# Optimization experiments

Hardware: AMD Instinct MI355X
Metric: run time of the kernel (lower is better)

The kernel has to match this reference:

```python
import jax, jax.numpy as jnp
import numpy as np
from jax import lax

B, C, H, W = 16, 128, 64, 64
AUX = 2 * 128 + 20 + 1  # hybrid: edge(128)+seg(128)+pred_edge(1)+pred_seg(20)
PATCHES = [(2, 2), (4, 4)]


def conv1x1(x, w, b):
    # w: [O, I]
    return jnp.einsum('bchw,oc->bohw', x, w) + b[None, :, None, None]


def conv3x3(x, w, b, pad, dil=1):
    y = lax.conv_general_dilated(x, w, (1, 1), [(pad, pad), (pad, pad)],
                                 rhs_dilation=(dil, dil),
                                 dimension_numbers=('NCHW', 'OIHW', 'NCHW'))
    return y + b[None, :, None, None]


def layernorm_chw(x, eps=1e-5):
    # LayerNorm over [C,H,W] per sample, no affine
    mu = x.mean(axis=(1, 2, 3), keepdims=True)
    var = ((x - mu) ** 2).mean(axis=(1, 2, 3), keepdims=True)
    return (x - mu) / jnp.sqrt(var + eps)


def adn(x, aux, ew, eb, sw, sb, bw, bb):
    a = conv1x1(aux, ew, eb)
    gamma = conv1x1(a, sw, sb)
    beta = conv1x1(jnp.concatenate([x, a], axis=1), bw, bb)
    return layernorm_chw(x) * gamma + beta


def window_attn(q, k, v, ph, pw):
    b, dk, h, w = q.shape
    oh, ow = h // ph, w // pw

    def patch(t):  # [b,dk,h,w] -> [b, oh*ow, dk*ph*pw]
        t = t.reshape(b, dk, oh, ph, ow, pw)
        return t.transpose(0, 2, 4, 1, 3, 5).reshape(b, oh * ow, dk * ph * pw)

    Q, K, V = patch(q), patch(k), patch(v)
    scale = 1.0 / jnp.sqrt(jnp.asarray(Q.shape[-1], Q.dtype))
    scores = jnp.einsum('bnd,bmd->bnm', Q, K) * scale
    y = jnp.einsum('bnm,bmd->bnd', jax.nn.softmax(scores, axis=-1), V)
    y = y.reshape(b, oh, ow, dk, ph, pw).transpose(0, 3, 1, 4, 2, 5).reshape(b, dk, h, w)
    return y


def mssa_forward(p):
    (x, edge, seg, pred_edge, pred_seg,
     q_w, q_b, k_w, k_b, v_w, v_b,
     d1_embed_w, d1_embed_b, d1_scale_w, d1_scale_b, d1_bias_w, d1_bias_b,
     d2_embed_w, d2_embed_b, d2_scale_w, d2_scale_b, d2_bias_w, d2_bias_b,
     sc_w, sc_b, bi1_w, bi1_b, bi2_w, bi2_b) = p

    aux = jnp.concatenate([edge, seg, pred_edge, pred_seg], axis=1)

    q = adn(conv1x1(x, q_w, q_b), aux, d1_embed_w, d1_embed_b, d1_scale_w, d1_scale_b, d1_bias_w, d1_bias_b)
    k = adn(conv1x1(x, k_w, k_b), aux, d1_embed_w, d1_embed_b, d1_scale_w, d1_scale_b, d1_bias_w, d1_bias_b)
    v = adn(conv1x1(x, v_w, v_b), aux, d1_embed_w, d1_embed_b, d1_scale_w, d1_scale_b, d1_bias_w, d1_bias_b)

    qs = jnp.split(q, len(PATCHES), axis=1)
    ks = jnp.split(k, len(PATCHES), axis=1)
    vs = jnp.split(v, len(PATCHES), axis=1)
    outs = [window_attn(qs[i], ks[i], vs[i], PATCHES[i][1], PATCHES[i][0]) for i in range(len(PATCHES))]

    mid = x + jnp.concatenate(outs, axis=1)
    o = adn(mid, aux, d2_embed_w, d2_embed_b, d2_scale_w, d2_scale_b, d2_bias_w, d2_bias_b)
    gamma = jnp.tanh(conv3x3(o, sc_w, sc_b, pad=1))
    beta = conv3x3(jax.nn.gelu(conv3x3(o, bi1_w, bi1_b, pad=2, dil=2), approximate=False), bi2_w, bi2_b, pad=1)
    return mid * gamma + beta


def setup_inputs() -> dict:
    key = jax.random.key(0)
    ks = iter(jax.random.split(key, 40))
    nrm = lambda shape, s=1.0: jax.random.normal(next(ks), shape, jnp.float32) * s
    P = 0.02  # param init scale
    inp = {
        'x': nrm((B, C, H, W)),
        'edge': nrm((B, 128, H, W)),
        'seg': nrm((B, 128, H, W)),
        'pred_edge': jax.random.uniform(next(ks), (B, 1, H, W), jnp.float32),
        'pred_seg': jax.random.uniform(next(ks), (B, 20, H, W), jnp.float32),
        'q_w': nrm((C, C), P), 'q_b': jnp.zeros((C,), jnp.float32),
        'k_w': nrm((C, C), P), 'k_b': jnp.zeros((C,), jnp.float32),
        'v_w': nrm((C, C), P), 'v_b': jnp.zeros((C,), jnp.float32),
        'd1_embed_w': nrm((C, AUX), P), 'd1_embed_b': jnp.zeros((C,), jnp.float32),
        'd1_scale_w': nrm((C, C), P), 'd1_scale_b': jnp.ones((C,), jnp.float32),
        'd1_bias_w': nrm((C, 2 * C), P), 'd1_bias_b': jnp.zeros((C,), jnp.float32),
        'd2_embed_w': nrm((C, AUX), P), 'd2_embed_b': jnp.zeros((C,), jnp.float32),
        'd2_scale_w': nrm((C, C), P), 'd2_scale_b': jnp.ones((C,), jnp.float32),
        'd2_bias_w': nrm((C, 2 * C), P), 'd2_bias_b': jnp.zeros((C,), jnp.float32),
        'sc_w': nrm((C, C, 3, 3), P), 'sc_b': jnp.zeros((C,), jnp.float32),
        'bi1_w': nrm((C, C, 3, 3), P), 'bi1_b': jnp.zeros((C,), jnp.float32),
        'bi2_w': nrm((C, C, 3, 3), P), 'bi2_b': jnp.zeros((C,), jnp.float32),
    }
    return inp


def reference(x, edge, seg, pred_edge, pred_seg,
              q_w, q_b, k_w, k_b, v_w, v_b,
              d1_embed_w, d1_embed_b, d1_scale_w, d1_scale_b, d1_bias_w, d1_bias_b,
              d2_embed_w, d2_embed_b, d2_scale_w, d2_scale_b, d2_bias_w, d2_bias_b,
              sc_w, sc_b, bi1_w, bi1_b, bi2_w, bi2_b):
    return mssa_forward((x, edge, seg, pred_edge, pred_seg,
                         q_w, q_b, k_w, k_b, v_w, v_b,
                         d1_embed_w, d1_embed_b, d1_scale_w, d1_scale_b, d1_bias_w, d1_bias_b,
                         d2_embed_w, d2_embed_b, d2_scale_w, d2_scale_b, d2_bias_w, d2_bias_b,
                         sc_w, sc_b, bi1_w, bi1_b, bi2_w, bi2_b))
```

## Files before the change

kernel.cpp:

```cpp
#include <hip/hip_runtime.h>
#include <cstdint>

typedef unsigned short ushort_t;
typedef unsigned int uint_t;
typedef __attribute__((ext_vector_type(8))) short short8;
typedef __attribute__((ext_vector_type(4))) float f32x4;

#define MFMA16(a, b, c) __builtin_amdgcn_mfma_f32_16x16x32_bf16((a), (b), (c), 0, 0, 0)
#define SWZ(c, r) ((((c) + ((r) >> 2)) & 3))
#define INV_N 1.9073486328125e-6f

struct P4 { ushort_t* p[4]; };
struct B4 { const float* b[4]; };

__device__ __forceinline__ ushort_t f2bf(float f) {
    uint_t u = __builtin_bit_cast(uint_t, f);
    u += 0x7FFFu + ((u >> 16) & 1u);
    return (ushort_t)(u >> 16);
}
__device__ __forceinline__ float bf2f(ushort_t h) {
    return __builtin_bit_cast(float, (uint_t)h << 16);
}

__global__ __launch_bounds__(256) void prep_w(
    ushort_t* wb, const float* qw, const float* kw, const float* vw,
    const float* ew1, const float* ew2, const float* sw1, const float* sw2,
    const float* bw1, const float* bw2,
    const float* scw, const float* b1w, const float* b2w)
{
    int idx = blockIdx.x * 256 + threadIdx.x;
    if (idx >= 663552) return;
    float v;
    if (idx < 49152) {
        int z = idx >> 14, r = idx & 16383;
        v = (z == 0 ? qw : z == 1 ? kw : vw)[r];
    } else if (idx < 122880) {
        int j = idx - 49152; int z = j / 36864; int jj = j - z * 36864;
        int o = jj / 288, k = jj - o * 288;
        v = (k < 277) ? (z ? ew2 : ew1)[o * 277 + k] : 0.f;
    } else if (idx < 155648) {
        int j = idx - 122880; int z = j >> 14;
        v = (z ? sw2 : sw1)[j & 16383];
    } else if (idx < 221184) {
        int j = idx - 155648; int z = j >> 15;
        v = (z ? bw2 : bw1)[j & 32767];
    } else {
        int j = idx - 221184;
        const float* src = j < 147456 ? scw : j < 294912 ? b1w : b2w;
        j = j % 147456;
        int tap = j >> 14, r = (j >> 7) & 127, c = j & 127;
        v = src[r * 1152 + c * 9 + tap];
    }
    wb[idx] = f2bf(v);
}

__global__ __launch_bounds__(256) void combine_w(ushort_t* wc, const ushort_t* wb)
{
    __shared__ float ews[128 * 33];
    __shared__ ushort_t Ws[128 * 130];
    int z = blockIdx.y, nt = blockIdx.x, n0 = nt * 32;
    int t = threadIdx.x;
    const ushort_t* wew = wb + 49152;
    const ushort_t* wsw = wb + 122880;
    const ushort_t* wbw = wb + 155648;
    const ushort_t* W; int wstr, wof;
    if (z == 0)      { W = wsw;         wstr = 128; wof = 0; }
    else if (z == 1) { W = wbw;         wstr = 256; wof = 128; }
    else if (z == 2) { W = wsw + 16384; wstr = 128; wof = 0; }
    else             { W = wbw + 32768; wstr = 256; wof = 128; }
    const ushort_t* E = wew + (z >= 2 ? 36864 : 0);
    for (int s = t; s < 16384; s += 256) {
        int c = s & 127, o = s >> 7;
        Ws[c * 130 + o] = W[o * wstr + wof + c];
    }
    for (int s = t; s < 4096; s += 256) {
        int c = s >> 5, n = s & 31;
        ews[c * 33 + n] = bf2f(E[c * 288 + n0 + n]);
    }
    __syncthreads();
    int o = t & 127, nh = t >> 7;
    float acc[16];
#pragma unroll
    for (int i = 0; i < 16; ++i) acc[i] = 0.f;
    for (int c = 0; c < 128; ++c) {
        float wv = bf2f(Ws[c * 130 + o]);
#pragma unroll
        for (int i = 0; i < 16; ++i) acc[i] += wv * ews[c * 33 + nh * 16 + i];
    }
#pragma unroll
    for (int i = 0; i < 16; ++i)
        wc[(size_t)(z * 128 + o) * 288 + n0 + nh * 16 + i] = f2bf(acc[i]);
}

__global__ __launch_bounds__(512) void combine_bias(
    float* bc, const float* sw1, const float* bw1, const float* sw2, const float* bw2,
    const float* eb1, const float* eb2, const float* sb1, const float* bb1,
    const float* sb2, const float* bb2)
{
    int t = threadIdx.x; int z = t >> 7, o = t & 127;
    const float* W; int wstr, wof; const float* eb; float add;
    if (z == 0)      { W = sw1; wstr = 128; wof = 0;   eb = eb1; add = sb1[o]; }
    else if (z == 1) { W = bw1; wstr = 256; wof = 128; eb = eb1; add = bb1[o]; }
    else if (z == 2) { W = sw2; wstr = 128; wof = 0;   eb = eb2; add = sb2[o]; }
    else             { W = bw2; wstr = 256; wof = 128; eb = eb2; add = bb2[o]; }
    float s = add;
    for (int c = 0; c < 128; ++c) s += W[o * wstr + wof + c] * eb[c];
    bc[t] = s;
}

__global__ __launch_bounds__(256) void transp_x(const float* __restrict__ x, ushort_t* __restrict__ xT)
{
    __shared__ ushort_t tile[64 * 130];
    int b = blockIdx.y, p0 = blockIdx.x * 64;
    int t = threadIdx.x;
#pragma unroll
    for (int i = 0; i < 8; ++i) {
        int s = t + i * 256;
        int c = s >> 4, p4 = (s & 15) * 4;
        float4 f = *(const float4*)(x + ((size_t)(b * 128 + c) << 12) + p0 + p4);
        tile[(p4 + 0) * 130 + c] = f2bf(f.x);
        tile[(p4 + 1) * 130 + c] = f2bf(f.y);
        tile[(p4 + 2) * 130 + c] = f2bf(f.z);
        tile[(p4 + 3) * 130 + c] = f2bf(f.w);
    }
    __syncthreads();
#pragma unroll
    for (int i = 0; i < 4; ++i) {
        int s = t + i * 256;
        int p = s >> 4, c8 = (s & 15) * 8;
        ushort_t v[8];
#pragma unroll
        for (int e = 0; e < 8; ++e) v[e] = tile[p * 130 + c8 + e];
        uint4 ov = {(uint_t)v[0] | ((uint_t)v[1] << 16), (uint_t)v[2] | ((uint_t)v[3] << 16),
                    (uint_t)v[4] | ((uint_t)v[5] << 16), (uint_t)v[6] | ((uint_t)v[7] << 16)};
        *(uint4*)(xT + ((size_t)(b * 4096) + p0 + p) * 128 + c8) = ov;
    }
}

__global__ __launch_bounds__(256) void transp_aux(const float* __restrict__ edge, const float* __restrict__ seg,
                                                  const float* __restrict__ pe, const float* __restrict__ ps,
                                                  ushort_t* __restrict__ auxT)
{
    __shared__ ushort_t tile[64 * 292];
    int b = blockIdx.y, p0 = blockIdx.x * 64;
    int t = threadIdx.x;
#pragma unroll
    for (int i = 0; i < 18; ++i) {
        int s = t + i * 256;
        int c = s >> 4, p4 = (s & 15) * 4;
        float4 f = {0.f, 0.f, 0.f, 0.f};
        if (c < 128)       f = *(const float4*)(edge + ((size_t)(b * 128 + c) << 12) + p0 + p4);
        else if (c < 256)  f = *(const float4*)(seg + ((size_t)(b * 128 + c - 128) << 12) + p0 + p4);
        else if (c == 256) f = *(const float4*)(pe + ((size_t)b << 12) + p0 + p4);
        else if (c < 277)  f = *(const float4*)(ps + ((size_t)(b * 20 + c - 257) << 12) + p0 + p4);
        tile[(p4 + 0) * 292 + c] = f2bf(f.x);
        tile[(p4 + 1) * 292 + c] = f2bf(f.y);
        tile[(p4 + 2) * 292 + c] = f2bf(f.z);
        tile[(p4 + 3) * 292 + c] = f2bf(f.w);
    }
    __syncthreads();
#pragma unroll
    for (int i = 0; i < 9; ++i) {
        int s = t + i * 256;
        int p = s / 36, c8 = (s % 36) * 8;
        ushort_t v[8];
#pragma unroll
        for (int e = 0; e < 8; ++e) v[e] = tile[p * 292 + c8 + e];
        uint4 ov = {(uint_t)v[0] | ((uint_t)v[1] << 16), (uint_t)v[2] | ((uint_t)v[3] << 16),
                    (uint_t)v[4] | ((uint_t)v[5] << 16), (uint_t)v[6] | ((uint_t)v[7] << 16)};
        *(uint4*)(auxT + ((size_t)(b * 4096) + p0 + p) * 288 + c8) = ov;
    }
}

template <int EP>
__global__ __launch_bounds__(256) void gemm_conv(
    const ushort_t* bA, int Kb1, size_t zBoff,
    const ushort_t* wA, int wstride, int wAperZ, int NK,
    B4 bias4, P4 out4, const ushort_t* gT, const ushort_t* betT,
    float* stats, int dostats)
{
    constexpr int LDSZ = (EP == 2) ? 33792 : 16448;
    __shared__ char lds[LDSZ];
    int b = blockIdx.y, bx = blockIdx.x, z = blockIdx.z;
    int t = threadIdx.x, lane = t & 63, w = t >> 6;
    int wm = w & 1, wn = w >> 1, lo = lane & 15, quad = lane >> 4;
    const ushort_t* wAz = wA + (wAperZ ? (size_t)z * 128 * wstride : 0);
    const ushort_t* bAz = bA + (size_t)z * zBoff;
    ushort_t* outp = out4.p[z];
    size_t bbase = (size_t)b * 4096;
    int y0 = 0, x0 = 0;
    if (EP == 2) { y0 = (bx >> 1) * 4; x0 = (bx & 1) * 32; }

    f32x4 acc[4][4];
#pragma unroll
    for (int i = 0; i < 4; ++i)
#pragma unroll
        for (int j = 0; j < 4; ++j) acc[i][j] = (f32x4){0.f, 0.f, 0.f, 0.f};

    int r0 = t >> 2, c0 = t & 3, r1 = r0 + 64;
    int gp0, gp1;
    if (EP == 2) {
        gp0 = (y0 + (r0 >> 5)) * 64 + x0 + (r0 & 31);
        gp1 = (y0 + (r1 >> 5)) * 64 + x0 + (r1 & 31);
    } else {
        gp0 = bx * 128 + r0;
        gp1 = bx * 128 + r1;
    }
    const ushort_t* bRow0 = bAz + (bbase + gp0) * Kb1;
    const ushort_t* bRow1 = bAz + (bbase + gp1) * Kb1;
    uint4 pfA0 = *(const uint4*)(wAz + (size_t)r0 * wstride + c0 * 8);
    uint4 pfA1 = *(const uint4*)(wAz + (size_t)r1 * wstride + c0 * 8);
    uint4 pfB0 = *(const uint4*)(bRow0 + c0 * 8);
    uint4 pfB1 = *(const uint4*)(bRow1 + c0 * 8);
    for (int ck = 0; ck < NK; ++ck) {
        __syncthreads();
        *(uint4*)(lds + r0 * 64 + SWZ(c0, r0) * 16) = pfA0;
        *(uint4*)(lds + r1 * 64 + SWZ(c0, r1) * 16) = pfA1;
        *(uint4*)(lds + 8192 + r0 * 64 + SWZ(c0, r0) * 16) = pfB0;
        *(uint4*)(lds + 8192 + r1 * 64 + SWZ(c0, r1) * 16) = pfB1;
        __syncthreads();
        if (ck + 1 < NK) {
            int k0 = (ck + 1) * 32;
            pfA0 = *(const uint4*)(wAz + (size_t)r0 * wstride + k0 + c0 * 8);
            pfA1 = *(const uint4*)(wAz + (size_t)r1 * wstride + k0 + c0 * 8);
            pfB0 = *(const uint4*)(bRow0 + k0 + c0 * 8);
            pfB1 = *(const uint4*)(bRow1 + k0 + c0 * 8);
        }
        short8 af[4];
#pragma unroll
        for (int mt = 0; mt < 4; ++mt) {
            int row = wm * 64 + mt * 16 + lo;
            af[mt] = *(const short8*)(lds + row * 64 + SWZ(quad, row) * 16);
        }
#pragma unroll
        for (int nt = 0; nt < 4; ++nt) {
            int n = wn * 64 + nt * 16 + lo;
            short8 bf = *(const short8*)(lds + 8192 + n * 64 + SWZ(quad, n) * 16);
#pragma unroll
            for (int mt = 0; mt < 4; ++mt) acc[mt][nt] = MFMA16(af[mt], bf, acc[mt][nt]);
        }
    }

    float mean = 0.f, rstd = 0.f;
    if (EP >= 2) {
        int slot = (EP == 3) ? 3 : z;
        float s0 = stats[(slot * 16 + b) * 2], s1 = stats[(slot * 16 + b) * 2 + 1];
        mean = s0 * INV_N;
        rstd = rsqrtf(fmaxf(s1 * INV_N - mean * mean, 0.f) + 1e-5f);
    }
    float lsum = 0.f, lss = 0.f;
    if (EP == 2) {
        __syncthreads();
        ushort_t* Cs = (ushort_t*)lds;
#pragma unroll
        for (int mt = 0; mt < 4; ++mt)
#pragma unroll
            for (int nt = 0; nt < 4; ++nt) {
                int oo0 = wm * 64 + mt * 16 + quad * 4;
                int pp = wn * 64 + nt * 16 + lo;
                int gp = (y0 + (pp >> 5)) * 64 + x0 + (pp & 31);
                size_t tbase = (bbase + gp) * 128 + oo0;
                ushort4 tv = *(const ushort4*)(bAz + tbase);
                ushort4 gv = *(const ushort4*)(gT + tbase);
                ushort4 bv = *(const ushort4*)(betT + tbase);
#pragma unroll
                for (int r = 0; r < 4; ++r) {
                    float v = acc[mt][nt][r] + bf2f((&bv.x)[r])
                            + (bf2f((&tv.x)[r]) - mean) * rstd * bf2f((&gv.x)[r]);
                    Cs[(oo0 + r) * 132 + pp] = f2bf(v);
                }
            }
        __syncthreads();
        if (z < 2) {
            for (int s = t; s < 1024; s += 256) {
                int n_l = s >> 5, fq = s & 31;
                int ypair = n_l >> 4, xp = n_l & 15;
                ushort_t tmp[8];
#pragma unroll
                for (int e = 0; e < 8; ++e) {
                    int f = fq * 8 + e;
                    int c = f >> 2, py = (f >> 1) & 1, px = f & 1;
                    tmp[e] = Cs[c * 132 + (ypair * 2 + py) * 32 + xp * 2 + px];
                }
                int n = ((y0 >> 1) + ypair) * 32 + (x0 >> 1) + xp;
                uint4 ov = {(uint_t)tmp[0] | ((uint_t)tmp[1] << 16), (uint_t)tmp[2] | ((uint_t)tmp[3] << 16),
                            (uint_t)tmp[4] | ((uint_t)tmp[5] << 16), (uint_t)tmp[6] | ((uint_t)tmp[7] << 16)};
                *(uint4*)(outp + ((size_t)(b * 1024 + n) << 8) + fq * 8) = ov;
            }
            for (int s = t; s < 1024; s += 256) {
                int n_l = s >> 7, fq = s & 127;
                ushort_t tmp[8];
#pragma unroll
                for (int e = 0; e < 8; ++e) {
                    int f = fq * 8 + e;
                    int c = f >> 4, py = (f >> 2) & 3, px = f & 3;
                    tmp[e] = Cs[(64 + c) * 132 + py * 32 + n_l * 4 + px];
                }
                int n = (y0 >> 2) * 16 + (x0 >> 2) + n_l;
                uint4 ov = {(uint_t)tmp[0] | ((uint_t)tmp[1] << 16), (uint_t)tmp[2] | ((uint_t)tmp[3] << 16),
                            (uint_t)tmp[4] | ((uint_t)tmp[5] << 16), (uint_t)tmp[6] | ((uint_t)tmp[7] << 16)};
                *(uint4*)(outp + 4194304u + ((size_t)(b * 256 + n) << 10) + fq * 8) = ov;
            }
        } else {
            for (int s = t; s < 2048; s += 256) {
                int f = s >> 3, j = s & 7;
                int ypair = j >> 2, xq = j & 3;
                int c = f >> 2, py = (f >> 1) & 1, px = f & 1;
                ushort_t tmp[4];
#pragma unroll
                for (int i2 = 0; i2 < 4; ++i2)
                    tmp[i2] = Cs[c * 132 + (ypair * 2 + py) * 32 + (xq * 4 + i2) * 2 + px];
                int m0 = ((y0 >> 1) + ypair) * 32 + (x0 >> 1) + xq * 4;
                uint2 ov = {(uint_t)tmp[0] | ((uint_t)tmp[1] << 16), (uint_t)tmp[2] | ((uint_t)tmp[3] << 16)};
                *(uint2*)(outp + ((size_t)(b * 256 + f) << 10) + m0) = ov;
            }
            for (int s = t; s < 2048; s += 256) {
                int f = s >> 1, j = s & 1;
                int c = f >> 4, py = (f >> 2) & 3, px = f & 3;
                ushort_t tmp[4];
#pragma unroll
                for (int i2 = 0; i2 < 4; ++i2)
                    tmp[i2] = Cs[(64 + c) * 132 + py * 32 + (j * 4 + i2) * 4 + px];
                int m0 = (y0 >> 2) * 16 + (x0 >> 2) + j * 4;
                uint2 ov = {(uint_t)tmp[0] | ((uint_t)tmp[1] << 16), (uint_t)tmp[2] | ((uint_t)tmp[3] << 16)};
                *(uint2*)(outp + 4194304u + ((size_t)(b * 1024 + f) << 8) + m0) = ov;
            }
        }
    } else {
#pragma unroll
        for (int mt = 0; mt < 4; ++mt)
#pragma unroll
            for (int nt = 0; nt < 4; ++nt) {
                int oo0 = wm * 64 + mt * 16 + quad * 4;
                int pp = wn * 64 + nt * 16 + lo;
                size_t tbase = (bbase + bx * 128 + pp) * 128 + oo0;
                float vv[4];
                if (EP == 0) {
#pragma unroll
                    for (int r = 0; r < 4; ++r) vv[r] = acc[mt][nt][r] + bias4.b[z][oo0 + r];
                    if (dostats) {
#pragma unroll
                        for (int r = 0; r < 4; ++r) { lsum += vv[r]; lss += vv[r] * vv[r]; }
                    }
                } else {
                    ushort4 tv = *(const ushort4*)(bAz + tbase);
                    ushort4 gv = *(const ushort4*)(gT + tbase);
                    ushort4 bv = *(const ushort4*)(betT + tbase);
#pragma unroll
                    for (int r = 0; r < 4; ++r)
                        vv[r] = acc[mt][nt][r] + bf2f((&bv.x)[r])
                              + (bf2f((&tv.x)[r]) - mean) * rstd * bf2f((&gv.x)[r]);
                }
                ushort4 st = {f2bf(vv[0]), f2bf(vv[1]), f2bf(vv[2]), f2bf(vv[3])};
                *(ushort4*)(outp + tbase) = st;
            }
    }
    if (EP == 0 && dostats) {
#pragma unroll
        for (int o2 = 32; o2 >= 1; o2 >>= 1) { lsum += __shfl_xor(lsum, o2); lss += __shfl_xor(lss, o2); }
        __syncthreads();
        float* red = (float*)lds;
        if (lane == 0) { red[w * 2] = lsum; red[w * 2 + 1] = lss; }
        __syncthreads();
        if (t == 0) {
            atomicAdd(&stats[(z * 16 + b) * 2], red[0] + red[2] + red[4] + red[6]);
            atomicAdd(&stats[(z * 16 + b) * 2 + 1], red[1] + red[3] + red[5] + red[7]);
        }
    }
}

template <int EP>
__global__ __launch_bounds__(256) void gemm_attn(
    const ushort_t* A, size_t aBS, const ushort_t* Bm, size_t bBS,
    int Ka, int NK, float scale,
    ushort_t* sout, size_t soBS, int soNb,
    const ushort_t* xT, ushort_t* midT, float* stats)
{
    constexpr int LDSZ = (EP >= 1) ? 33792 : 16448;
    __shared__ char lds[LDSZ];
    int b = blockIdx.z, my = blockIdx.y, nx = blockIdx.x;
    int t = threadIdx.x, lane = t & 63, w = t >> 6;
    int wm = w & 1, wn = w >> 1, lo = lane & 15, quad = lane >> 4;

    f32x4 acc[4][4];
#pragma unroll
    for (int i = 0; i < 4; ++i)
#pragma unroll
        for (int j = 0; j < 4; ++j) acc[i][j] = (f32x4){0.f, 0.f, 0.f, 0.f};

    const ushort_t* Ab = A + b * aBS + (size_t)(my * 128) * Ka;
    const ushort_t* Bb = Bm + b * bBS + (size_t)(nx * 128) * Ka;
    int r0 = t >> 2, c0 = t & 3, r1 = r0 + 64;
    uint4 pfA0 = *(const uint4*)(Ab + (size_t)r0 * Ka + c0 * 8);
    uint4 pfA1 = *(const uint4*)(Ab + (size_t)r1 * Ka + c0 * 8);
    uint4 pfB0 = *(const uint4*)(Bb + (size_t)r0 * Ka + c0 * 8);
    uint4 pfB1 = *(const uint4*)(Bb + (size_t)r1 * Ka + c0 * 8);
    for (int ck = 0; ck < NK; ++ck) {
        __syncthreads();
        *(uint4*)(lds + r0 * 64 + SWZ(c0, r0) * 16) = pfA0;
        *(uint4*)(lds + r1 * 64 + SWZ(c0, r1) * 16) = pfA1;
        *(uint4*)(lds + 8192 + r0 * 64 + SWZ(c0, r0) * 16) = pfB0;
        *(uint4*)(lds + 8192 + r1 * 64 + SWZ(c0, r1) * 16) = pfB1;
        __syncthreads();
        if (ck + 1 < NK) {
            int k0 = (ck + 1) * 32;
            pfA0 = *(const uint4*)(Ab + (size_t)r0 * Ka + k0 + c0 * 8);
            pfA1 = *(const uint4*)(Ab + (size_t)r1 * Ka + k0 + c0 * 8);
            pfB0 = *(const uint4*)(Bb + (size_t)r0 * Ka + k0 + c0 * 8);
            pfB1 = *(const uint4*)(Bb + (size_t)r1 * Ka + k0 + c0 * 8);
        }
        short8 af[4];
#pragma unroll
        for (int mt = 0; mt < 4; ++mt) {
            int row = wm * 64 + mt * 16 + lo;
            af[mt] = *(const short8*)(lds + row * 64 + SWZ(quad, row) * 16);
        }
#pragma unroll
        for (int nt = 0; nt < 4; ++nt) {
            int n = wn * 64 + nt * 16 + lo;
            short8 bf = *(const short8*)(lds + 8192 + n * 64 + SWZ(quad, n) * 16);
#pragma unroll
            for (int mt = 0; mt < 4; ++mt) acc[mt][nt] = MFMA16(af[mt], bf, acc[mt][nt]);
        }
    }

    if (EP == 0) {
#pragma unroll
        for (int mt = 0; mt < 4; ++mt)
#pragma unroll
            for (int nt = 0; nt < 4; ++nt)
#pragma unroll
                for (int reg = 0; reg < 4; ++reg) {
                    int rr = my * 128 + wm * 64 + mt * 16 + quad * 4 + reg;
                    int cc = nx * 128 + wn * 64 + nt * 16 + lo;
                    sout[(size_t)b * soBS + (size_t)rr * soNb + cc] = f2bf(acc[mt][nt][reg] * scale);
                }
        return;
    }
    __syncthreads();
    ushort_t* Cs = (ushort_t*)lds;
#pragma unroll
    for (int mt = 0; mt < 4; ++mt)
#pragma unroll
        for (int nt = 0; nt < 4; ++nt)
#pragma unroll
            for (int reg = 0; reg < 4; ++reg) {
                int r_l = wm * 64 + mt * 16 + quad * 4 + reg;
                int c_l = wn * 64 + nt * 16 + lo;
                Cs[r_l * 132 + c_l] = f2bf(acc[mt][nt][reg]);
            }
    __syncthreads();
    float lsum = 0.f, lss = 0.f;
    for (int s = t; s < 4096; s += 256) {
        int sp, r_l, cbase, pybit, pxbit;
        if (EP == 1) {
            int sp_l = s >> 3, cj = s & 7;
            int y_l = sp_l >> 6, xv = sp_l & 63;
            r_l = (y_l >> 1) * 32 + (xv >> 1);
            sp = (my * 8 + y_l) * 64 + xv;
            cbase = nx * 32 + cj * 4;
            pybit = (y_l & 1) * 2 + (xv & 1);
            pxbit = 4;
        } else {
            int sp_l = s >> 1, cj = s & 1;
            int y_l = sp_l >> 6, xv = sp_l & 63;
            r_l = (y_l >> 2) * 16 + (xv >> 2);
            sp = (my * 32 + y_l) * 64 + xv;
            cbase = 64 + nx * 8 + cj * 4;
            pybit = (y_l & 3) * 4 + (xv & 3);
            pxbit = 16;
        }
        size_t base = ((size_t)(b * 4096) + sp) * 128 + cbase;
        ushort4 xv4 = *(const ushort4*)(xT + base);
        int c_l0 = (EP == 1) ? (cbase - nx * 32) * 4 + pybit : (cbase - 64 - nx * 8) * 16 + pybit;
        ushort_t o4[4];
#pragma unroll
        for (int ci = 0; ci < 4; ++ci) {
            float vm = bf2f(Cs[r_l * 132 + c_l0 + ci * pxbit]) + bf2f((&xv4.x)[ci]);
            o4[ci] = f2bf(vm);
            lsum += vm; lss += vm * vm;
        }
        ushort4 st = {o4[0], o4[1], o4[2], o4[3]};
        *(ushort4*)(midT + base) = st;
    }
#pragma unroll
    for (int o2 = 32; o2 >= 1; o2 >>= 1) { lsum += __shfl_xor(lsum, o2); lss += __shfl_xor(lss, o2); }
    __syncthreads();
    float* red = (float*)lds;
    if (lane == 0) { red[w * 2] = lsum; red[w * 2 + 1] = lss; }
    __syncthreads();
    if (t == 0) {
        atomicAdd(&stats[(3 * 16 + b) * 2], red[0] + red[2] + red[4] + red[6]);
        atomicAdd(&stats[(3 * 16 + b) * 2 + 1], red[1] + red[3] + red[5] + red[7]);
    }
}

__global__ __launch_bounds__(256) void softmax_k(ushort_t* SP)
{
    int wid = blockIdx.x * 4 + (threadIdx.x >> 6);
    int lane = threadIdx.x & 63;
    ushort_t* row;
    int PL;
    if (wid < 16384) { row = SP + ((size_t)wid << 10); PL = 16; }
    else { int r2 = wid - 16384; row = SP + 16777216u + ((size_t)r2 << 8); PL = 4; }
    float v[16];
    float mx = -1e30f;
    for (int i = 0; i < PL; ++i) { v[i] = bf2f(row[lane + (i << 6)]); mx = fmaxf(mx, v[i]); }
#pragma unroll
    for (int o = 32; o >= 1; o >>= 1) mx = fmaxf(mx, __shfl_xor(mx, o));
    float sum = 0.f;
    for (int i = 0; i < PL; ++i) { v[i] = __expf(v[i] - mx); sum += v[i]; }
#pragma unroll
    for (int o = 32; o >= 1; o >>= 1) sum += __shfl_xor(sum, o);
    float inv = 1.f / sum;
    for (int i = 0; i < PL; ++i) row[lane + (i << 6)] = f2bf(v[i] * inv);
}

__global__ __launch_bounds__(512) void conv3x3_dual(
    const ushort_t* __restrict__ inT, const ushort_t* __restrict__ wtA, const ushort_t* __restrict__ wtB,
    const float* __restrict__ biasA, const float* __restrict__ biasB,
    ushort_t* __restrict__ outA, ushort_t* __restrict__ outB)
{
    __shared__ char lds[24576 + 8 * 68 * 64];
    char* Braw = lds + 24576;
    int b = blockIdx.y, z = blockIdx.z;
    int dil = 1 + z;
    int NRr = 4 + 2 * dil;
    const ushort_t* wt = z ? wtB : wtA;
    const float* bias = z ? biasB : biasA;
    ushort_t* out = z ? outB : outA;
    int y0 = blockIdx.x * 4;
    int t = threadIdx.x, lane = t & 63, w = t >> 6;
    int wm = w & 1, wn = w >> 1, lo = lane & 15, quad = lane >> 4;

    f32x4 acc[4][4];
#pragma unroll
    for (int i = 0; i < 4; ++i)
#pragma unroll
        for (int j = 0; j < 4; ++j) acc[i][j] = (f32x4){0.f, 0.f, 0.f, 0.f};

    for (int cc = 0; cc < 4; ++cc) {
        __syncthreads();
        int NSLOT = NRr * 68 * 4;
        for (int s = t; s < NSLOT; s += 512) {
            int c4 = s & 3;
            int pr = s >> 2;
            int xx = pr % 68, rr = pr / 68;
            int ys = y0 - dil + rr;
            int ix = xx - dil;
            uint4 v = {0u, 0u, 0u, 0u};
            if (ys >= 0 && ys < 64 && (unsigned)ix < 64u)
                v = *(const uint4*)(inT + (size_t)(b * 4096 + ys * 64 + ix) * 128 + cc * 32 + c4 * 8);
            *(uint4*)(Braw + pr * 64 + SWZ(c4, pr) * 16) = v;
        }
        for (int ky = 0; ky < 3; ++ky) {
            __syncthreads();
            for (int s = t; s < 1536; s += 512) {
                int kx = s >> 9, r = (s >> 2) & 127, c = s & 3;
                uint4 v = *(const uint4*)(wt + ((size_t)((ky * 3 + kx) * 128 + r) << 7) + cc * 32 + c * 8);
                *(uint4*)(lds + kx * 8192 + r * 64 + SWZ(c, r) * 16) = v;
            }
            __syncthreads();
#pragma unroll
            for (int kx = 0; kx < 3; ++kx) {
                short8 af[4];
#pragma unroll
                for (int mt = 0; mt < 4; ++mt) {
                    int row = wm * 64 + mt * 16 + lo;
                    af[mt] = *(const short8*)(lds + kx * 8192 + row * 64 + SWZ(quad, row) * 16);
                }
#pragma unroll
                for (int nt = 0; nt < 4; ++nt) {
                    int n = wn * 64 + nt * 16 + lo;
                    int pr = ((n >> 6) + ky * dil) * 68 + (n & 63) + kx * dil;
                    short8 bf = *(const short8*)(Braw + pr * 64 + SWZ(quad, pr) * 16);
#pragma unroll
                    for (int mt = 0; mt < 4; ++mt) acc[mt][nt] = MFMA16(af[mt], bf, acc[mt][nt]);
                }
            }
        }
    }
#pragma unroll
    for (int mt = 0; mt < 4; ++mt)
#pragma unroll
        for (int nt = 0; nt < 4; ++nt) {
            int oo0 = wm * 64 + mt * 16 + quad * 4;
            int pp = wn * 64 + nt * 16 + lo;
            int sp = (y0 + (pp >> 6)) * 64 + (pp & 63);
            size_t tbase = ((size_t)(b * 4096) + sp) * 128 + oo0;
            ushort4 st;
#pragma unroll
            for (int r = 0; r < 4; ++r) {
                float v = acc[mt][nt][r] + bias[oo0 + r];
                if (z == 0) v = tanhf(v);
                else        v = 0.5f * v * (1.f + erff(v * 0.70710678118654752f));
                (&st.x)[r] = f2bf(v);
            }
            *(ushort4*)(out + tbase) = st;
        }
}

__global__ __launch_bounds__(512) void conv3x3_final(
    const ushort_t* __restrict__ inT, const ushort_t* __restrict__ wt, const float* __restrict__ bias,
    float* __restrict__ out, const ushort_t* __restrict__ midT, const ushort_t* __restrict__ g3T)
{
    __shared__ char lds[24576 + 6 * 68 * 64];
    char* Braw = lds + 24576;
    int b = blockIdx.y;
    int y0 = blockIdx.x * 4;
    int t = threadIdx.x, lane = t & 63, w = t >> 6;
    int wm = w & 1, wn = w >> 1, lo = lane & 15, quad = lane >> 4;

    f32x4 acc[4][4];
#pragma unroll
    for (int i = 0; i < 4; ++i)
#pragma unroll
        for (int j = 0; j < 4; ++j) acc[i][j] = (f32x4){0.f, 0.f, 0.f, 0.f};

    for (int cc = 0; cc < 4; ++cc) {
        __syncthreads();
        for (int s = t; s < 1632; s += 512) {
            int c4 = s & 3;
            int pr = s >> 2;
            int xx = pr % 68, rr = pr / 68;
            int ys = y0 - 1 + rr;
            int ix = xx - 1;
            uint4 v = {0u, 0u, 0u, 0u};
            if (ys >= 0 && ys < 64 && (unsigned)ix < 64u)
                v = *(const uint4*)(inT + (size_t)(b * 4096 + ys * 64 + ix) * 128 + cc * 32 + c4 * 8);
            *(uint4*)(Braw + pr * 64 + SWZ(c4, pr) * 16) = v;
        }
        for (int ky = 0; ky < 3; ++ky) {
            __syncthreads();
            for (int s = t; s < 1536; s += 512) {
                int kx = s >> 9, r = (s >> 2) & 127, c = s & 3;
                uint4 v = *(const uint4*)(wt + ((size_t)((ky * 3 + kx) * 128 + r) << 7) + cc * 32 + c * 8);
                *(uint4*)(lds + kx * 8192 + r * 64 + SWZ(c, r) * 16) = v;
            }
            __syncthreads();
#pragma unroll
            for (int kx = 0; kx < 3; ++kx) {
                short8 af[4];
#pragma unroll
                for (int mt = 0; mt < 4; ++mt) {
                    int row = wm * 64 + mt * 16 + lo;
                    af[mt] = *(const short8*)(lds + kx * 8192 + row * 64 + SWZ(quad, row) * 16);
                }
#pragma unroll
                for (int nt = 0; nt < 4; ++nt) {
                    int n = wn * 64 + nt * 16 + lo;
                    int pr = ((n >> 6) + ky) * 68 + (n & 63) + kx;
                    short8 bf = *(const short8*)(Braw + pr * 64 + SWZ(quad, pr) * 16);
#pragma unroll
                    for (int mt = 0; mt < 4; ++mt) acc[mt][nt] = MFMA16(af[mt], bf, acc[mt][nt]);
                }
            }
        }
    }
#pragma unroll
    for (int mt = 0; mt < 4; ++mt)
#pragma unroll
        for (int nt = 0; nt < 4; ++nt) {
            int oo0 = wm * 64 + mt * 16 + quad * 4;
            int pp = wn * 64 + nt * 16 + lo;
            int sp = (y0 + (pp >> 6)) * 64 + (pp & 63);
            size_t tbase = ((size_t)(b * 4096) + sp) * 128 + oo0;
            ushort4 mv = *(const ushort4*)(midT + tbase);
            ushort4 gv = *(const ushort4*)(g3T + tbase);
#pragma unroll
            for (int r = 0; r < 4; ++r) {
                int oo = oo0 + r;
                size_t off = ((size_t)(b * 128 + oo) << 12) + sp;
                out[off] = bf2f((&mv.x)[r]) * bf2f((&gv.x)[r]) + acc[mt][nt][r] + bias[oo];
            }
        }
}

extern "C" void kernel_launch(void* const* d_in, const int* in_sizes, int n_in,
                              void* d_out, int out_size, void* d_ws, size_t ws_size,
                              hipStream_t stream)
{
    const float* x    = (const float*)d_in[0];
    const float* edge = (const float*)d_in[1];
    const float* seg  = (const float*)d_in[2];
    const float* pe   = (const float*)d_in[3];
    const float* ps   = (const float*)d_in[4];
    const float* q_w  = (const float*)d_in[5];  const float* q_b  = (const float*)d_in[6];
    const float* k_w  = (const float*)d_in[7];  const float* k_b  = (const float*)d_in[8];
    const float* v_w  = (const float*)d_in[9];  const float* v_b  = (const float*)d_in[10];
    const float* d1_ew = (const float*)d_in[11]; const float* d1_eb = (const float*)d_in[12];
    const float* d1_sw = (const float*)d_in[13]; const float* d1_sb = (const float*)d_in[14];
    const float* d1_bw = (const float*)d_in[15]; const float* d1_bb = (const float*)d_in[16];
    const float* d2_ew = (const float*)d_in[17]; const float* d2_eb = (const float*)d_in[18];
    const float* d2_sw = (const float*)d_in[19]; const float* d2_sb = (const float*)d_in[20];
    const float* d2_bw = (const float*)d_in[21]; const float* d2_bb = (const float*)d_in[22];
    const float* sc_w  = (const float*)d_in[23]; const float* sc_b  = (const float*)d_in[24];
    const float* bi1_w = (const float*)d_in[25]; const float* bi1_b = (const float*)d_in[26];
    const float* bi2_w = (const float*)d_in[27]; const float* bi2_b = (const float*)d_in[28];

    char* ws = (char*)d_ws;
    ushort_t* wb = (ushort_t*)ws;
    ushort_t* wc = (ushort_t*)(ws + 1327360);
    float* bc    = (float*)(ws + 1622272);
    float* stats = (float*)(ws + 1624320);
    char* RA = ws + 1703936;
    char* RB = RA + 37748736;
    char* RC = RB + 16777216;
    char* RD = RC + 50331648;
    char* RE = RD + 16777216;
    char* RF = RE + 16777216;
    char* RG = RF + 16777216;
    char* RH = RG + 16777216;
    char* RI = RH + 33554432;

    ushort_t* auxT = (ushort_t*)RA;
    ushort_t* SP0  = (ushort_t*)RA;
    ushort_t* xT   = (ushort_t*)RB;
    ushort_t* q0T  = (ushort_t*)RC;
    ushort_t* midT = (ushort_t*)RC;
    ushort_t* oT   = (ushort_t*)(RC + 16777216);
    ushort_t* g1   = (ushort_t*)RD;
    ushort_t* g3   = (ushort_t*)RD;
    ushort_t* betA1= (ushort_t*)RE;
    ushort_t* g2   = (ushort_t*)RF;
    ushort_t* betA2= (ushort_t*)RG;
    ushort_t* Qp   = (ushort_t*)RH;
    ushort_t* Kp   = Qp + 8388608;
    ushort_t* VT   = (ushort_t*)RI;
    ushort_t* tT   = (ushort_t*)RI;
    const size_t ZB = 8388608;

    dim3 blk(256);

    hipMemsetAsync(stats, 0, 512, stream);
    prep_w<<<2592, blk, 0, stream>>>(wb, q_w, k_w, v_w, d1_ew, d2_ew, d1_sw, d2_sw, d1_bw, d2_bw, sc_w, bi1_w, bi2_w);
    combine_bias<<<1, 512, 0, stream>>>(bc, d1_sw, d1_bw, d2_sw, d2_bw, d1_eb, d2_eb, d1_sb, d1_bb, d2_sb, d2_bb);
    combine_w<<<dim3(9, 4), blk, 0, stream>>>(wc, wb);
    transp_x<<<dim3(64, 16), blk, 0, stream>>>(x, xT);
    transp_aux<<<dim3(64, 16), blk, 0, stream>>>(edge, seg, pe, ps, auxT);

    gemm_conv<0><<<dim3(32, 16, 4), blk, 0, stream>>>(auxT, 288, 0, wc, 288, 1, 9,
        B4{{bc, bc + 128, bc + 256, bc + 384}}, P4{{g1, betA1, g2, betA2}}, nullptr, nullptr, stats, 0);
    gemm_conv<0><<<dim3(32, 16, 3), blk, 0, stream>>>(xT, 128, 0, wb, 128, 1, 4,
        B4{{q_b, k_b, v_b, nullptr}}, P4{{q0T, q0T + ZB, q0T + 2 * ZB, nullptr}}, nullptr, nullptr, stats, 1);
    gemm_conv<2><<<dim3(32, 16, 3), blk, 0, stream>>>(q0T, 128, ZB, wb + 155648, 256, 0, 4,
        B4{{nullptr, nullptr, nullptr, nullptr}}, P4{{Qp, Kp, VT, nullptr}}, g1, betA1, stats, 0);

    gemm_attn<0><<<dim3(8, 8, 16), blk, 0, stream>>>(Qp, 262144, Kp, 262144, 256, 8, 0.0625f,
        SP0, 1048576, 1024, nullptr, nullptr, stats);
    gemm_attn<0><<<dim3(2, 2, 16), blk, 0, stream>>>(Qp + 4194304, 262144, Kp + 4194304, 262144, 1024, 32, 0.03125f,
        SP0 + 16777216, 65536, 256, nullptr, nullptr, stats);
    softmax_k<<<5120, blk, 0, stream>>>(SP0);
    gemm_attn<1><<<dim3(2, 8, 16), blk, 0, stream>>>(SP0, 1048576, VT, 262144, 1024, 32, 1.f,
        nullptr, 0, 0, xT, midT, stats);
    gemm_attn<2><<<dim3(8, 2, 16), blk, 0, stream>>>(SP0 + 16777216, 65536, VT + 4194304, 262144, 256, 8, 1.f,
        nullptr, 0, 0, xT, midT, stats);

    gemm_conv<3><<<dim3(32, 16, 1), blk, 0, stream>>>(midT, 128, 0, wb + 155648 + 32768, 256, 0, 4,
        B4{{nullptr, nullptr, nullptr, nullptr}}, P4{{oT, nullptr, nullptr, nullptr}}, g2, betA2, stats, 0);

    conv3x3_dual<<<dim3(16, 16, 2), dim3(512), 0, stream>>>(oT, wb + 221184, wb + 368640, sc_b, bi1_b, g3, tT);
    conv3x3_final<<<dim3(16, 16), dim3(512), 0, stream>>>(tT, wb + 516096, bi2_b, (float*)d_out, midT, g3);
}
```

Measured before the change: 694.5 us.

## Stage all nine conv taps per channel chunk and enlarge dual-conv row tile

Both 3x3 conv kernels now load the weights for all nine taps of a 32-channel chunk into LDS at once, so each chunk needs one barrier pair instead of one per ky row. The dual conv kernel also doubles its tile to 8 output rows with 1024-thread blocks, which halves the block count and spreads the halo and weight loads over more output rows. The cost is much larger LDS use (about 72KB of weights plus the halo tile), which caps how many blocks fit on a CU, and fewer blocks in the grid.

```diff
diff --git a/kernel.cpp b/kernel.cpp
--- a/kernel.cpp
+++ b/kernel.cpp
@@ -516,22 +516,22 @@
     for (int i = 0; i < PL; ++i) row[lane + (i << 6)] = f2bf(v[i] * inv);
 }
 
-__global__ __launch_bounds__(512) void conv3x3_dual(
+__global__ __launch_bounds__(1024) void conv3x3_dual(
     const ushort_t* __restrict__ inT, const ushort_t* __restrict__ wtA, const ushort_t* __restrict__ wtB,
     const float* __restrict__ biasA, const float* __restrict__ biasB,
     ushort_t* __restrict__ outA, ushort_t* __restrict__ outB)
 {
-    __shared__ char lds[24576 + 8 * 68 * 64];
-    char* Braw = lds + 24576;
+    __shared__ char lds[73728 + 12 * 68 * 64];
+    char* Braw = lds + 73728;
     int b = blockIdx.y, z = blockIdx.z;
     int dil = 1 + z;
-    int NRr = 4 + 2 * dil;
+    int NRr = 8 + 2 * dil;
     const ushort_t* wt = z ? wtB : wtA;
     const float* bias = z ? biasB : biasA;
     ushort_t* out = z ? outB : outA;
-    int y0 = blockIdx.x * 4;
+    int y0 = blockIdx.x * 8;
     int t = threadIdx.x, lane = t & 63, w = t >> 6;
-    int wm = w & 1, wn = w >> 1, lo = lane & 15, quad = lane >> 4;
+    int wm = w & 1, wr = w >> 1, lo = lane & 15, quad = lane >> 4;
 
     f32x4 acc[4][4];
 #pragma unroll
@@ -540,9 +540,14 @@
         for (int j = 0; j < 4; ++j) acc[i][j] = (f32x4){0.f, 0.f, 0.f, 0.f};
 
     for (int cc = 0; cc < 4; ++cc) {
-        __syncthreads();
-        int NSLOT = NRr * 68 * 4;
-        for (int s = t; s < NSLOT; s += 512) {
+        if (cc) __syncthreads();
+        for (int s = t; s < 4608; s += 1024) {
+            int tap = s >> 9, r = (s >> 2) & 127, c = s & 3;
+            uint4 v = *(const uint4*)(wt + ((size_t)(tap * 128 + r) << 7) + cc * 32 + c * 8);
+            *(uint4*)(lds + tap * 8192 + r * 64 + SWZ(c, r) * 16) = v;
+        }
+        int NSLOT = NRr * 272;
+        for (int s = t; s < NSLOT; s += 1024) {
             int c4 = s & 3;
             int pr = s >> 2;
             int xx = pr % 68, rr = pr / 68;
@@ -553,30 +558,22 @@
                 v = *(const uint4*)(inT + (size_t)(b * 4096 + ys * 64 + ix) * 128 + cc * 32 + c4 * 8);
             *(uint4*)(Braw + pr * 64 + SWZ(c4, pr) * 16) = v;
         }
-        for (int ky = 0; ky < 3; ++ky) {
-            __syncthreads();
-            for (int s = t; s < 1536; s += 512) {
-                int kx = s >> 9, r = (s >> 2) & 127, c = s & 3;
-                uint4 v = *(const uint4*)(wt + ((size_t)((ky * 3 + kx) * 128 + r) << 7) + cc * 32 + c * 8);
-                *(uint4*)(lds + kx * 8192 + r * 64 + SWZ(c, r) * 16) = v;
-            }
-            __syncthreads();
-#pragma unroll
-            for (int kx = 0; kx < 3; ++kx) {
-                short8 af[4];
-#pragma unroll
-                for (int mt = 0; mt < 4; ++mt) {
-                    int row = wm * 64 + mt * 16 + lo;
-                    af[mt] = *(const short8*)(lds + kx * 8192 + row * 64 + SWZ(quad, row) * 16);
-                }
-#pragma unroll
-                for (int nt = 0; nt < 4; ++nt) {
-                    int n = wn * 64 + nt * 16 + lo;
-                    int pr = ((n >> 6) + ky * dil) * 68 + (n & 63) + kx * dil;
-                    short8 bf = *(const short8*)(Braw + pr * 64 + SWZ(quad, pr) * 16);
-#pragma unroll
-                    for (int mt = 0; mt < 4; ++mt) acc[mt][nt] = MFMA16(af[mt], bf, acc[mt][nt]);
-                }
+        __syncthreads();
+#pragma unroll
+        for (int tap = 0; tap < 9; ++tap) {
+            int ky = tap / 3, kx = tap % 3;
+            short8 af[4];
+#pragma unroll
+            for (int mt = 0; mt < 4; ++mt) {
+                int row = wm * 64 + mt * 16 + lo;
+                af[mt] = *(const short8*)(lds + tap * 8192 + row * 64 + SWZ(quad, row) * 16);
+            }
+#pragma unroll
+            for (int nt = 0; nt < 4; ++nt) {
+                int pr = (wr + ky * dil) * 68 + nt * 16 + lo + kx * dil;
+                short8 bf = *(const short8*)(Braw + pr * 64 + SWZ(quad, pr) * 16);
+#pragma unroll
+                for (int mt = 0; mt < 4; ++mt) acc[mt][nt] = MFMA16(af[mt], bf, acc[mt][nt]);
             }
         }
     }
@@ -585,8 +582,8 @@
 #pragma unroll
         for (int nt = 0; nt < 4; ++nt) {
             int oo0 = wm * 64 + mt * 16 + quad * 4;
-            int pp = wn * 64 + nt * 16 + lo;
-            int sp = (y0 + (pp >> 6)) * 64 + (pp & 63);
+            int col = nt * 16 + lo;
+            int sp = (y0 + wr) * 64 + col;
             size_t tbase = ((size_t)(b * 4096) + sp) * 128 + oo0;
             ushort4 st;
 #pragma unroll
@@ -604,12 +601,12 @@
     const ushort_t* __restrict__ inT, const ushort_t* __restrict__ wt, const float* __restrict__ bias,
     float* __restrict__ out, const ushort_t* __restrict__ midT, const ushort_t* __restrict__ g3T)
 {
-    __shared__ char lds[24576 + 6 * 68 * 64];
-    char* Braw = lds + 24576;
+    __shared__ char lds[73728 + 6 * 68 * 64];
+    char* Braw = lds + 73728;
     int b = blockIdx.y;
     int y0 = blockIdx.x * 4;
     int t = threadIdx.x, lane = t & 63, w = t >> 6;
-    int wm = w & 1, wn = w >> 1, lo = lane & 15, quad = lane >> 4;
+    int wm = w & 1, wr = w >> 1, lo = lane & 15, quad = lane >> 4;
 
     f32x4 acc[4][4];
 #pragma unroll
@@ -618,7 +615,12 @@
         for (int j = 0; j < 4; ++j) acc[i][j] = (f32x4){0.f, 0.f, 0.f, 0.f};
 
     for (int cc = 0; cc < 4; ++cc) {
-        __syncthreads();
+        if (cc) __syncthreads();
+        for (int s = t; s < 4608; s += 512) {
+            int tap = s >> 9, r = (s >> 2) & 127, c = s & 3;
+            uint4 v = *(const uint4*)(wt + ((size_t)(tap * 128 + r) << 7) + cc * 32 + c * 8);
+            *(uint4*)(lds + tap * 8192 + r * 64 + SWZ(c, r) * 16) = v;
+        }
         for (int s = t; s < 1632; s += 512) {
             int c4 = s & 3;
             int pr = s >> 2;
@@ -630,30 +632,22 @@
                 v = *(const uint4*)(inT + (size_t)(b * 4096 + ys * 64 + ix) * 128 + cc * 32 + c4 * 8);
             *(uint4*)(Braw + pr * 64 + SWZ(c4, pr) * 16) = v;
         }
-        for (int ky = 0; ky < 3; ++ky) {
-            __syncthreads();
-            for (int s = t; s < 1536; s += 512) {
-                int kx = s >> 9, r = (s >> 2) & 127, c = s & 3;
-                uint4 v = *(const uint4*)(wt + ((size_t)((ky * 3 + kx) * 128 + r) << 7) + cc * 32 + c * 8);
-                *(uint4*)(lds + kx * 8192 + r * 64 + SWZ(c, r) * 16) = v;
-            }
-            __syncthreads();
-#pragma unroll
-            for (int kx = 0; kx < 3; ++kx) {
-                short8 af[4];
-#pragma unroll
-                for (int mt = 0; mt < 4; ++mt) {
-                    int row = wm * 64 + mt * 16 + lo;
-                    af[mt] = *(const short8*)(lds + kx * 8192 + row * 64 + SWZ(quad, row) * 16);
-                }
-#pragma unroll
-                for (int nt = 0; nt < 4; ++nt) {
-                    int n = wn * 64 + nt * 16 + lo;
-                    int pr = ((n >> 6) + ky) * 68 + (n & 63) + kx;
-                    short8 bf = *(const short8*)(Braw + pr * 64 + SWZ(quad, pr) * 16);
-#pragma unroll
-                    for (int mt = 0; mt < 4; ++mt) acc[mt][nt] = MFMA16(af[mt], bf, acc[mt][nt]);
-                }
+        __syncthreads();
+#pragma unroll
+        for (int tap = 0; tap < 9; ++tap) {
+            int ky = tap / 3, kx = tap % 3;
+            short8 af[4];
+#pragma unroll
+            for (int mt = 0; mt < 4; ++mt) {
+                int row = wm * 64 + mt * 16 + lo;
+                af[mt] = *(const short8*)(lds + tap * 8192 + row * 64 + SWZ(quad, row) * 16);
+            }
+#pragma unroll
+            for (int nt = 0; nt < 4; ++nt) {
+                int pr = (wr + ky) * 68 + nt * 16 + lo + kx;
+                short8 bf = *(const short8*)(Braw + pr * 64 + SWZ(quad, pr) * 16);
+#pragma unroll
+                for (int mt = 0; mt < 4; ++mt) acc[mt][nt] = MFMA16(af[mt], bf, acc[mt][nt]);
             }
         }
     }
@@ -662,8 +656,8 @@
 #pragma unroll
         for (int nt = 0; nt < 4; ++nt) {
             int oo0 = wm * 64 + mt * 16 + quad * 4;
-            int pp = wn * 64 + nt * 16 + lo;
-            int sp = (y0 + (pp >> 6)) * 64 + (pp & 63);
+            int col = nt * 16 + lo;
+            int sp = (y0 + wr) * 64 + col;
             size_t tbase = ((size_t)(b * 4096) + sp) * 128 + oo0;
             ushort4 mv = *(const ushort4*)(midT + tbase);
             ushort4 gv = *(const ushort4*)(g3T + tbase);
@@ -759,6 +753,6 @@
     gemm_conv<3><<<dim3(32, 16, 1), blk, 0, stream>>>(midT, 128, 0, wb + 155648 + 32768, 256, 0, 4,
         B4{{nullptr, nullptr, nullptr, nullptr}}, P4{{oT, nullptr, nullptr, nullptr}}, g2, betA2, stats, 0);
 
-    conv3x3_dual<<<dim3(16, 16, 2), dim3(512), 0, stream>>>(oT, wb + 221184, wb + 368640, sc_b, bi1_b, g3, tT);
+    conv3x3_dual<<<dim3(8, 16, 2), dim3(1024), 0, stream>>>(oT, wb + 221184, wb + 368640, sc_b, bi1_b, g3, tT);
     conv3x3_final<<<dim3(16, 16), dim3(512), 0, stream>>>(tT, wb + 516096, bi2_b, (float*)d_out, midT, g3);
 }
```

After: 680.0 us. 2.1% less time.
